# Kernel tuning notes

Hardware: AMD Instinct MI355X
Metric: run time of the kernel (lower is better)

The kernel has to match this reference:

```python
import jax, jax.numpy as jnp
import numpy as np

B, L, H, VOC, OUT = 64, 512, 64, 32000, 5


def setup_inputs() -> dict:
    key = jax.random.key(0)
    ks = jax.random.split(key, 7)
    tokens = jax.random.randint(ks[0], (B, L), 0, VOC, dtype=jnp.int32)
    embed = jax.random.normal(ks[1], (VOC, H), dtype=jnp.float32) * 0.1
    V = jax.random.normal(ks[2], (H, 2 * H, 2 * H), dtype=jnp.float32) * 0.05
    W = jax.random.normal(ks[3], (2 * H, H), dtype=jnp.float32) * 0.05
    b = jax.random.normal(ks[4], (1, H), dtype=jnp.float32) * 0.05
    Wout = jax.random.normal(ks[5], (H, OUT), dtype=jnp.float32) * 0.05
    bout = jax.random.normal(ks[6], (OUT,), dtype=jnp.float32) * 0.05
    return {"tokens": tokens, "embed": embed, "V": V, "W": W, "b": b,
            "Wout": Wout, "bout": bout}


def _combine(c, V, W, b):
    # c: [B, N, 2H] concatenated (left, right) children.
    # xVx[b,n,i] = c[b,n] @ V[i] @ c[b,n]^T  (RNTN bilinear term)
    xVx = jnp.einsum('bnp,ipq,bnq->bni', c, V, c)
    Wx = jnp.einsum('bnp,ph->bnh', c, W)
    return jnp.tanh(xVx + Wx + b)  # b broadcasts [1,H] -> [B,N,H]


def reference(tokens, embed, V, W, b, Wout, bout):
    # Leaves: embedding lookup, [B, L, H]
    nodes = embed[tokens]
    # Complete binary tree: combine adjacent pairs level by level
    # (fixed log2(L)=9 levels -> static shapes, jit friendly)
    while nodes.shape[1] > 1:
        left = nodes[:, 0::2]   # [B, N/2, H]
        right = nodes[:, 1::2]  # [B, N/2, H]
        c = jnp.concatenate([left, right], axis=-1)  # [B, N/2, 2H]
        nodes = _combine(c, V, W, b)
    root = nodes[:, 0]  # [B, H]
    logits = root @ Wout + bout
    return jax.nn.log_softmax(logits, axis=-1)
```

## Files before the change

### kernel.cpp

```cpp
#include <hip/hip_runtime.h>
#include <cmath>

static constexpr int kB = 64, kL = 512, kH = 64, kH2 = 128, kOut = 5, kVoc = 32000;

typedef short bf16x8 __attribute__((ext_vector_type(8)));
typedef short s16x4  __attribute__((ext_vector_type(4)));
typedef float f32x4  __attribute__((ext_vector_type(4)));

__device__ __forceinline__ unsigned short f2bf(float f) {
  unsigned u = __float_as_uint(f);
  unsigned r = (u + 0x7FFFu + ((u >> 16) & 1u)) >> 16;
  return (unsigned short)r;
}

__device__ __forceinline__ float bf2f(unsigned short u) {
  return __uint_as_float(((unsigned)u) << 16);
}

__global__ void prep_k(const float* __restrict__ V, const float* __restrict__ W,
                       const float* __restrict__ embed,
                       unsigned short* __restrict__ vhi, unsigned short* __restrict__ wt,
                       unsigned short* __restrict__ ebf) {
  int idx = blockIdx.x * 256 + threadIdx.x;
  if (idx < kH * kH2 * kH2) { vhi[idx] = f2bf(V[idx]); return; }
  idx -= kH * kH2 * kH2;
  if (idx < kH * kH2) {
    int i = idx >> 7, p = idx & 127;
    wt[idx] = f2bf(W[p * kH + i]);
    return;
  }
  idx -= kH * kH2;
  if (idx < kVoc * kH) ebf[idx] = f2bf(embed[idx]);
}

template<bool FIRST>
__global__ __launch_bounds__(256) void combine2_k(
    const unsigned short* __restrict__ inbf, const int* __restrict__ tokens,
    const unsigned short* __restrict__ vhi, const unsigned short* __restrict__ wt,
    const float* __restrict__ bias, unsigned short* __restrict__ outbf,
    int M, int IS)
{
  __shared__ unsigned short Vs[2][kH2 * kH2];
  __shared__ float res[128 * 17];

  const int t = threadIdx.x;
  const int lane = t & 63, w = t >> 6;
  const int c = lane & 15, q = lane >> 4;
  const int m0 = (int)blockIdx.x * 128;
  const int i0 = (int)blockIdx.y * IS;
  const int Mrows = (M < 128) ? M : 128;
  const bool has_rows = (w * 32) < Mrows;

  bf16x8 bh[2][4];
  f32x4  Cred[2][8];

  if (has_rows) {
    #pragma unroll
    for (int mt = 0; mt < 2; ++mt) {
      int m = m0 + w * 32 + mt * 16 + c;
      const unsigned short* brow = nullptr;
      int tokA = 0, tokB = 0;
      if (FIRST) {
        int b = m >> 8, j = m & 255;
        tokA = tokens[b * kL + 2 * j];
        tokB = tokens[b * kL + 2 * j + 1];
      } else {
        brow = inbf + (size_t)m * kH2;
      }
      #pragma unroll
      for (int ks = 0; ks < 4; ++ks) {
        int q0 = ks * 32 + q * 8;
        const unsigned short* bsrc = FIRST
            ? (inbf + (size_t)(q0 < 64 ? tokA : tokB) * kH + (q0 & 63))
            : (brow + q0);
        bh[mt][ks] = *(const bf16x8*)bsrc;
      }
      #pragma unroll
      for (int pt = 0; pt < 8; ++pt) {
        int p0 = pt * 16 + q * 4;
        const unsigned short* csrc = FIRST
            ? (inbf + (size_t)(p0 < 64 ? tokA : tokB) * kH + (p0 & 63))
            : (brow + p0);
        s16x4 cv = *(const s16x4*)csrc;
        f32x4 cr;
        cr[0] = bf2f((unsigned short)cv[0]);
        cr[1] = bf2f((unsigned short)cv[1]);
        cr[2] = bf2f((unsigned short)cv[2]);
        cr[3] = bf2f((unsigned short)cv[3]);
        Cred[mt][pt] = cr;
      }
    }
    {
      int irow = i0 + c; if (irow > 63) irow = 63;
      f32x4 ah0 = {0.f,0.f,0.f,0.f}, ah1 = ah0;
      #pragma unroll
      for (int ks = 0; ks < 4; ++ks) {
        bf16x8 a = *(const bf16x8*)(wt + (size_t)irow * kH2 + ks * 32 + q * 8);
        ah0 = __builtin_amdgcn_mfma_f32_16x16x32_bf16(a, bh[0][ks], ah0, 0, 0, 0);
        ah1 = __builtin_amdgcn_mfma_f32_16x16x32_bf16(a, bh[1][ks], ah1, 0, 0, 0);
      }
      #pragma unroll
      for (int reg = 0; reg < 4; ++reg) {
        int ii = q * 4 + reg;
        if (ii < IS) {
          float bv = bias[i0 + ii];
          res[(w * 32 + c) * 17 + ii]      = ah0[reg] + bv;
          res[(w * 32 + 16 + c) * 17 + ii] = ah1[reg] + bv;
        }
      }
    }
  }

  auto stageV = [&](int i, int buf) {
    const unsigned short* vsrc = vhi + (size_t)i * (kH2 * kH2);
    #pragma unroll
    for (int r = 0; r < 8; ++r) {
      int chunk = w * 512 + r * 64 + lane;
      int p  = chunk >> 4;
      int pc = chunk & 15;
      int cc = pc ^ (p & 7);
      const unsigned short* g = vsrc + p * kH2 + cc * 8;
      __builtin_amdgcn_global_load_lds(
          (const __attribute__((address_space(1))) unsigned int*)g,
          (__attribute__((address_space(3))) unsigned int*)
              ((char*)&Vs[buf][0] + (size_t)(w * 512 + r * 64) * 16),
          16, 0, 0);
    }
  };

  auto computeIC = [&](int ic, int buf) {
    const char* vbase = (const char*)&Vs[buf][0];
    float g0 = 0.f, g1 = 0.f;
    for (int pt = 0; pt < 8; ++pt) {
      f32x4 a0 = {0.f,0.f,0.f,0.f}, a2 = a0;
      #pragma unroll
      for (int ks = 0; ks < 4; ++ks) {
        int p  = pt * 16 + c;
        int cc = (ks * 4 + q) ^ (p & 7);
        bf16x8 vf = *(const bf16x8*)(vbase + (size_t)p * 256 + cc * 16);
        a0 = __builtin_amdgcn_mfma_f32_16x16x32_bf16(vf, bh[0][ks], a0, 0, 0, 0);
        a2 = __builtin_amdgcn_mfma_f32_16x16x32_bf16(vf, bh[1][ks], a2, 0, 0, 0);
      }
      f32x4 cr0 = Cred[0][pt], cr1 = Cred[1][pt];
      g0 = fmaf(cr0[0], a0[0], g0); g0 = fmaf(cr0[1], a0[1], g0);
      g0 = fmaf(cr0[2], a0[2], g0); g0 = fmaf(cr0[3], a0[3], g0);
      g1 = fmaf(cr1[0], a2[0], g1); g1 = fmaf(cr1[1], a2[1], g1);
      g1 = fmaf(cr1[2], a2[2], g1); g1 = fmaf(cr1[3], a2[3], g1);
    }
    g0 += __shfl_xor(g0, 16); g0 += __shfl_xor(g0, 32);
    g1 += __shfl_xor(g1, 16); g1 += __shfl_xor(g1, 32);
    if (q == 0)      res[(w * 32 + c) * 17 + ic]      += g0;
    else if (q == 1) res[(w * 32 + 16 + c) * 17 + ic] += g1;
  };

  if (IS >= 2) {
    stageV(i0, 0); stageV(i0 + 1, 1);
    __syncthreads();
    for (int icp = 0; icp < IS; icp += 2) {
      if (has_rows) {
        computeIC(icp, 0);
        computeIC(icp + 1, 1);
      }
      __syncthreads();
      if (icp + 2 < IS) {
        stageV(i0 + icp + 2, 0); stageV(i0 + icp + 3, 1);
        __syncthreads();
      }
    }
  } else {
    stageV(i0, 0);
    __syncthreads();
    if (has_rows) computeIC(0, 0);
    __syncthreads();
  }

  const int sh = __builtin_ctz(IS);
  for (int idx = t; idx < Mrows * IS; idx += 256) {
    int m = idx >> sh, ii = idx & (IS - 1);
    outbf[(size_t)(m0 + m) * kH + i0 + ii] = f2bf(tanhf(res[m * 17 + ii]));
  }
}

__global__ void head_k(const unsigned short* __restrict__ root,
                       const float* __restrict__ Wout,
                       const float* __restrict__ bout,
                       float* __restrict__ out) {
  int b = threadIdx.x;
  float l[kOut];
  #pragma unroll
  for (int o = 0; o < kOut; ++o) l[o] = bout[o];
  for (int h = 0; h < kH; ++h) {
    float r = bf2f(root[b * kH + h]);
    #pragma unroll
    for (int o = 0; o < kOut; ++o) l[o] = fmaf(r, Wout[h * kOut + o], l[o]);
  }
  float mx = l[0];
  #pragma unroll
  for (int o = 1; o < kOut; ++o) mx = fmaxf(mx, l[o]);
  float s = 0.f;
  #pragma unroll
  for (int o = 0; o < kOut; ++o) s += expf(l[o] - mx);
  float lse = logf(s);
  #pragma unroll
  for (int o = 0; o < kOut; ++o) out[b * kOut + o] = l[o] - mx - lse;
}

extern "C" void kernel_launch(void* const* d_in, const int* in_sizes, int n_in,
                              void* d_out, int out_size, void* d_ws, size_t ws_size,
                              hipStream_t stream) {
  const int*   tokens = (const int*)  d_in[0];
  const float* embed  = (const float*)d_in[1];
  const float* V      = (const float*)d_in[2];
  const float* W      = (const float*)d_in[3];
  const float* bias   = (const float*)d_in[4];
  const float* Wout   = (const float*)d_in[5];
  const float* bout   = (const float*)d_in[6];
  float* out = (float*)d_out;

  char* ws = (char*)d_ws;
  unsigned short* vhi = (unsigned short*)ws;
  unsigned short* wt  = (unsigned short*)(ws + 2097152);
  unsigned short* ebf = (unsigned short*)(ws + 2097152 + 16384);
  unsigned short* bfA = (unsigned short*)(ws + 2097152 + 16384 + 4194304);
  unsigned short* bfB = (unsigned short*)(ws + 2097152 + 16384 + 4194304 + 2097152);

  int nprep = kH * kH2 * kH2 + kH * kH2 + kVoc * kH;
  prep_k<<<dim3((nprep + 255) / 256), 256, 0, stream>>>(V, W, embed, vhi, wt, ebf);

  const unsigned short* cur = nullptr;
  unsigned short* nxt = bfA;
  bool first = true;
  for (int Nout = 256; Nout >= 1; Nout >>= 1) {
    int M = kB * Nout;
    int gx = (M + 127) / 128;
    int IS = gx / 8; if (IS < 1) IS = 1; if (IS > 16) IS = 16;
    dim3 grid(gx, 64 / IS);
    if (first)
      combine2_k<true ><<<grid, 256, 0, stream>>>(ebf, tokens, vhi, wt, bias, nxt, M, IS);
    else
      combine2_k<false><<<grid, 256, 0, stream>>>(cur, nullptr, vhi, wt, bias, nxt, M, IS);
    first = false;
    cur = nxt;
    nxt = (nxt == bfA) ? bfB : bfA;
  }
  head_k<<<1, 64, 0, stream>>>(cur, Wout, bout, out);
}
```

Measured before the change: 206.1 us.

## Single-buffer V slice in LDS and halve output-column split per block

Shrinks shared memory by staging one V slice at a time instead of two, and shrinks the result buffer to 8 columns. The per-block output-column count (IS) is capped at 8 and derived from gx/16, so the grid launches twice as many y-blocks on large levels. The goal is higher occupancy and more parallel blocks, in exchange for more synchronisation barriers per block and more redundant loading of child rows across blocks.

Result: slower. 239.4 us (+16.2%).

```diff
diff --git a/kernel.cpp b/kernel.cpp
--- a/kernel.cpp
+++ b/kernel.cpp
@@ -40,8 +40,8 @@
     const float* __restrict__ bias, unsigned short* __restrict__ outbf,
     int M, int IS)
 {
-  __shared__ unsigned short Vs[2][kH2 * kH2];
-  __shared__ float res[128 * 17];
+  __shared__ unsigned short Vs[kH2 * kH2];
+  __shared__ float res[128 * 9];
 
   const int t = threadIdx.x;
   const int lane = t & 63, w = t >> 6;
@@ -104,14 +104,14 @@
         int ii = q * 4 + reg;
         if (ii < IS) {
           float bv = bias[i0 + ii];
-          res[(w * 32 + c) * 17 + ii]      = ah0[reg] + bv;
-          res[(w * 32 + 16 + c) * 17 + ii] = ah1[reg] + bv;
+          res[(w * 32 + c) * 9 + ii]      = ah0[reg] + bv;
+          res[(w * 32 + 16 + c) * 9 + ii] = ah1[reg] + bv;
         }
       }
     }
   }
 
-  auto stageV = [&](int i, int buf) {
+  auto stageV = [&](int i) {
     const unsigned short* vsrc = vhi + (size_t)i * (kH2 * kH2);
     #pragma unroll
     for (int r = 0; r < 8; ++r) {
@@ -123,13 +123,13 @@
       __builtin_amdgcn_global_load_lds(
           (const __attribute__((address_space(1))) unsigned int*)g,
           (__attribute__((address_space(3))) unsigned int*)
-              ((char*)&Vs[buf][0] + (size_t)(w * 512 + r * 64) * 16),
+              ((char*)&Vs[0] + (size_t)(w * 512 + r * 64) * 16),
           16, 0, 0);
     }
   };
 
-  auto computeIC = [&](int ic, int buf) {
-    const char* vbase = (const char*)&Vs[buf][0];
+  auto computeIC = [&](int ic) {
+    const char* vbase = (const char*)&Vs[0];
     float g0 = 0.f, g1 = 0.f;
     for (int pt = 0; pt < 8; ++pt) {
       f32x4 a0 = {0.f,0.f,0.f,0.f}, a2 = a0;
@@ -149,35 +149,22 @@
     }
     g0 += __shfl_xor(g0, 16); g0 += __shfl_xor(g0, 32);
     g1 += __shfl_xor(g1, 16); g1 += __shfl_xor(g1, 32);
-    if (q == 0)      res[(w * 32 + c) * 17 + ic]      += g0;
-    else if (q == 1) res[(w * 32 + 16 + c) * 17 + ic] += g1;
+    if (q == 0)      res[(w * 32 + c) * 9 + ic]      += g0;
+    else if (q == 1) res[(w * 32 + 16 + c) * 9 + ic] += g1;
   };
 
-  if (IS >= 2) {
-    stageV(i0, 0); stageV(i0 + 1, 1);
+  stageV(i0);
+  __syncthreads();
+  for (int ic = 0; ic < IS; ++ic) {
+    if (has_rows) computeIC(ic);
     __syncthreads();
-    for (int icp = 0; icp < IS; icp += 2) {
-      if (has_rows) {
-        computeIC(icp, 0);
-        computeIC(icp + 1, 1);
-      }
-      __syncthreads();
-      if (icp + 2 < IS) {
-        stageV(i0 + icp + 2, 0); stageV(i0 + icp + 3, 1);
-        __syncthreads();
-      }
-    }
-  } else {
-    stageV(i0, 0);
-    __syncthreads();
-    if (has_rows) computeIC(0, 0);
-    __syncthreads();
+    if (ic + 1 < IS) { stageV(i0 + ic + 1); __syncthreads(); }
   }
 
   const int sh = __builtin_ctz(IS);
   for (int idx = t; idx < Mrows * IS; idx += 256) {
     int m = idx >> sh, ii = idx & (IS - 1);
-    outbf[(size_t)(m0 + m) * kH + i0 + ii] = f2bf(tanhf(res[m * 17 + ii]));
+    outbf[(size_t)(m0 + m) * kH + i0 + ii] = f2bf(tanhf(res[m * 9 + ii]));
   }
 }
 
@@ -233,7 +220,7 @@
   for (int Nout = 256; Nout >= 1; Nout >>= 1) {
     int M = kB * Nout;
     int gx = (M + 127) / 128;
-    int IS = gx / 8; if (IS < 1) IS = 1; if (IS > 16) IS = 16;
+    int IS = gx / 16; if (IS < 1) IS = 1; if (IS > 8) IS = 8;
     dim3 grid(gx, 64 / IS);
     if (first)
       combine2_k<true ><<<grid, 256, 0, stream>>>(ebf, tokens, vhi, wt, bias, nxt, M, IS);
```

## Double rows per block to 256 for greater V reuse per LDS stage

Applied to the files above, without the earlier changes.

Each block now handles 256 rows, with four 16-row M tiles per wave instead of two, so every V slice staged into LDS feeds twice as many MFMAs. The per-block output-channel split is capped at 8, which roughly halves total V staging traffic across the grid. Child values are now kept as packed bf16 and converted to float inside the inner loop, saving registers at the cost of extra conversion ALU work. The risks are higher register pressure, lower occupancy, and fewer blocks on the small upper tree levels.

Result: slower. 257.7 us (+25.1%).

```diff
diff --git a/kernel.cpp b/kernel.cpp
--- a/kernel.cpp
+++ b/kernel.cpp
@@ -41,23 +41,23 @@
     int M, int IS)
 {
   __shared__ unsigned short Vs[2][kH2 * kH2];
-  __shared__ float res[128 * 17];
+  __shared__ float res[256 * 9];
 
   const int t = threadIdx.x;
   const int lane = t & 63, w = t >> 6;
   const int c = lane & 15, q = lane >> 4;
-  const int m0 = (int)blockIdx.x * 128;
+  const int m0 = (int)blockIdx.x * 256;
   const int i0 = (int)blockIdx.y * IS;
-  const int Mrows = (M < 128) ? M : 128;
-  const bool has_rows = (w * 32) < Mrows;
-
-  bf16x8 bh[2][4];
-  f32x4  Cred[2][8];
+  const int Mrows = (M < 256) ? M : 256;
+  const bool has_rows = (w * 64) < Mrows;
+
+  bf16x8 bh[4][4];
+  s16x4  cb[4][8];
 
   if (has_rows) {
     #pragma unroll
-    for (int mt = 0; mt < 2; ++mt) {
-      int m = m0 + w * 32 + mt * 16 + c;
+    for (int mt = 0; mt < 4; ++mt) {
+      int m = m0 + w * 64 + mt * 16 + c;
       const unsigned short* brow = nullptr;
       int tokA = 0, tokB = 0;
       if (FIRST) {
@@ -81,31 +81,29 @@
         const unsigned short* csrc = FIRST
             ? (inbf + (size_t)(p0 < 64 ? tokA : tokB) * kH + (p0 & 63))
             : (brow + p0);
-        s16x4 cv = *(const s16x4*)csrc;
-        f32x4 cr;
-        cr[0] = bf2f((unsigned short)cv[0]);
-        cr[1] = bf2f((unsigned short)cv[1]);
-        cr[2] = bf2f((unsigned short)cv[2]);
-        cr[3] = bf2f((unsigned short)cv[3]);
-        Cred[mt][pt] = cr;
+        cb[mt][pt] = *(const s16x4*)csrc;
       }
     }
     {
       int irow = i0 + c; if (irow > 63) irow = 63;
-      f32x4 ah0 = {0.f,0.f,0.f,0.f}, ah1 = ah0;
+      f32x4 ah0 = {0.f,0.f,0.f,0.f}, ah1 = ah0, ah2 = ah0, ah3 = ah0;
       #pragma unroll
       for (int ks = 0; ks < 4; ++ks) {
         bf16x8 a = *(const bf16x8*)(wt + (size_t)irow * kH2 + ks * 32 + q * 8);
         ah0 = __builtin_amdgcn_mfma_f32_16x16x32_bf16(a, bh[0][ks], ah0, 0, 0, 0);
         ah1 = __builtin_amdgcn_mfma_f32_16x16x32_bf16(a, bh[1][ks], ah1, 0, 0, 0);
+        ah2 = __builtin_amdgcn_mfma_f32_16x16x32_bf16(a, bh[2][ks], ah2, 0, 0, 0);
+        ah3 = __builtin_amdgcn_mfma_f32_16x16x32_bf16(a, bh[3][ks], ah3, 0, 0, 0);
       }
       #pragma unroll
       for (int reg = 0; reg < 4; ++reg) {
         int ii = q * 4 + reg;
         if (ii < IS) {
           float bv = bias[i0 + ii];
-          res[(w * 32 + c) * 17 + ii]      = ah0[reg] + bv;
-          res[(w * 32 + 16 + c) * 17 + ii] = ah1[reg] + bv;
+          res[(w * 64 +  0 + c) * 9 + ii] = ah0[reg] + bv;
+          res[(w * 64 + 16 + c) * 9 + ii] = ah1[reg] + bv;
+          res[(w * 64 + 32 + c) * 9 + ii] = ah2[reg] + bv;
+          res[(w * 64 + 48 + c) * 9 + ii] = ah3[reg] + bv;
         }
       }
     }
@@ -130,27 +128,40 @@
 
   auto computeIC = [&](int ic, int buf) {
     const char* vbase = (const char*)&Vs[buf][0];
-    float g0 = 0.f, g1 = 0.f;
+    float g0 = 0.f, g1 = 0.f, g2 = 0.f, g3 = 0.f;
     for (int pt = 0; pt < 8; ++pt) {
-      f32x4 a0 = {0.f,0.f,0.f,0.f}, a2 = a0;
+      int p = pt * 16 + c;
+      f32x4 a0 = {0.f,0.f,0.f,0.f}, a1 = a0, a2 = a0, a3 = a0;
       #pragma unroll
       for (int ks = 0; ks < 4; ++ks) {
-        int p  = pt * 16 + c;
         int cc = (ks * 4 + q) ^ (p & 7);
         bf16x8 vf = *(const bf16x8*)(vbase + (size_t)p * 256 + cc * 16);
         a0 = __builtin_amdgcn_mfma_f32_16x16x32_bf16(vf, bh[0][ks], a0, 0, 0, 0);
-        a2 = __builtin_amdgcn_mfma_f32_16x16x32_bf16(vf, bh[1][ks], a2, 0, 0, 0);
-      }
-      f32x4 cr0 = Cred[0][pt], cr1 = Cred[1][pt];
-      g0 = fmaf(cr0[0], a0[0], g0); g0 = fmaf(cr0[1], a0[1], g0);
-      g0 = fmaf(cr0[2], a0[2], g0); g0 = fmaf(cr0[3], a0[3], g0);
-      g1 = fmaf(cr1[0], a2[0], g1); g1 = fmaf(cr1[1], a2[1], g1);
-      g1 = fmaf(cr1[2], a2[2], g1); g1 = fmaf(cr1[3], a2[3], g1);
+        a1 = __builtin_amdgcn_mfma_f32_16x16x32_bf16(vf, bh[1][ks], a1, 0, 0, 0);
+        a2 = __builtin_amdgcn_mfma_f32_16x16x32_bf16(vf, bh[2][ks], a2, 0, 0, 0);
+        a3 = __builtin_amdgcn_mfma_f32_16x16x32_bf16(vf, bh[3][ks], a3, 0, 0, 0);
+      }
+      #pragma unroll
+      for (int mt = 0; mt < 4; ++mt) {
+        s16x4 cv = cb[mt][pt];
+        float c0 = bf2f((unsigned short)cv[0]);
+        float c1 = bf2f((unsigned short)cv[1]);
+        float c2 = bf2f((unsigned short)cv[2]);
+        float c3 = bf2f((unsigned short)cv[3]);
+        f32x4 av = (mt == 0) ? a0 : (mt == 1) ? a1 : (mt == 2) ? a2 : a3;
+        float* gp = (mt == 0) ? &g0 : (mt == 1) ? &g1 : (mt == 2) ? &g2 : &g3;
+        float gg = *gp;
+        gg = fmaf(c0, av[0], gg); gg = fmaf(c1, av[1], gg);
+        gg = fmaf(c2, av[2], gg); gg = fmaf(c3, av[3], gg);
+        *gp = gg;
+      }
     }
     g0 += __shfl_xor(g0, 16); g0 += __shfl_xor(g0, 32);
     g1 += __shfl_xor(g1, 16); g1 += __shfl_xor(g1, 32);
-    if (q == 0)      res[(w * 32 + c) * 17 + ic]      += g0;
-    else if (q == 1) res[(w * 32 + 16 + c) * 17 + ic] += g1;
+    g2 += __shfl_xor(g2, 16); g2 += __shfl_xor(g2, 32);
+    g3 += __shfl_xor(g3, 16); g3 += __shfl_xor(g3, 32);
+    float gq = (q == 0) ? g0 : (q == 1) ? g1 : (q == 2) ? g2 : g3;
+    res[(w * 64 + q * 16 + c) * 9 + ic] += gq;
   };
 
   if (IS >= 2) {
@@ -177,7 +188,7 @@
   const int sh = __builtin_ctz(IS);
   for (int idx = t; idx < Mrows * IS; idx += 256) {
     int m = idx >> sh, ii = idx & (IS - 1);
-    outbf[(size_t)(m0 + m) * kH + i0 + ii] = f2bf(tanhf(res[m * 17 + ii]));
+    outbf[(size_t)(m0 + m) * kH + i0 + ii] = f2bf(tanhf(res[m * 9 + ii]));
   }
 }
 
@@ -232,8 +243,8 @@
   bool first = true;
   for (int Nout = 256; Nout >= 1; Nout >>= 1) {
     int M = kB * Nout;
-    int gx = (M + 127) / 128;
-    int IS = gx / 8; if (IS < 1) IS = 1; if (IS > 16) IS = 16;
+    int gx = (M + 255) / 256;
+    int IS = gx / 8; if (IS < 1) IS = 1; if (IS > 8) IS = 8;
     dim3 grid(gx, 64 / IS);
     if (first)
       combine2_k<true ><<<grid, 256, 0, stream>>>(ebf, tokens, vhi, wt, bias, nxt, M, IS);
```
